# Kernel tuning notes

Measured on AMD Instinct MI355X. Metric: run time of the kernel, lower is better.

The kernel has to match this reference:

```python
import jax, jax.numpy as jnp
import numpy as np

N, E, HEADS = 50000, 800000, 4
IN_C, HID_C, OUT_C = 128, 64, 40
WIDTH = HEADS * HID_C  # 256
NEG_SLOPE = 0.2
BN_EPS = 1e-5


def setup_inputs() -> dict:
    key = jax.random.key(0)
    ks = jax.random.split(key, 16)
    s = 0.05
    inp = {
        "x": jax.random.normal(ks[0], (N, IN_C), jnp.float32),
        "edge_index": jax.random.randint(ks[1], (2, E), 0, N, jnp.int32),
        # layer 0: in -> (heads, hid), concat
        "W0": jax.random.normal(ks[2], (IN_C, WIDTH), jnp.float32) * s,
        "a_src0": jax.random.normal(ks[3], (HEADS, HID_C), jnp.float32) * s,
        "a_dst0": jax.random.normal(ks[4], (HEADS, HID_C), jnp.float32) * s,
        "b0": jnp.zeros((WIDTH,), jnp.float32),
        "g0": jnp.ones((WIDTH,), jnp.float32),
        "beta0": jnp.zeros((WIDTH,), jnp.float32),
        # layer 1: width -> (heads, hid), concat
        "W1": jax.random.normal(ks[5], (WIDTH, WIDTH), jnp.float32) * s,
        "a_src1": jax.random.normal(ks[6], (HEADS, HID_C), jnp.float32) * s,
        "a_dst1": jax.random.normal(ks[7], (HEADS, HID_C), jnp.float32) * s,
        "b1": jnp.zeros((WIDTH,), jnp.float32),
        "g1": jnp.ones((WIDTH,), jnp.float32),
        "beta1": jnp.zeros((WIDTH,), jnp.float32),
        # layer 2: width -> (heads, out), mean over heads (concat=False)
        "W2": jax.random.normal(ks[8], (WIDTH, HEADS * OUT_C), jnp.float32) * s,
        "a_src2": jax.random.normal(ks[9], (HEADS, OUT_C), jnp.float32) * s,
        "a_dst2": jax.random.normal(ks[10], (HEADS, OUT_C), jnp.float32) * s,
        "b2": jnp.zeros((OUT_C,), jnp.float32),
    }
    return inp


def _gat_layer(x, W, a_src, a_dst, b, src, dst, out_c, concat):
    # x: [N, F_in]; W: [F_in, HEADS*out_c]
    h = (x @ W).reshape(N, HEADS, out_c)              # [N, H, C]
    e_src = jnp.sum(h * a_src, axis=-1)               # [N, H]
    e_dst = jnp.sum(h * a_dst, axis=-1)               # [N, H]
    e = jax.nn.leaky_relu(e_src[src] + e_dst[dst], NEG_SLOPE)  # [E', H]
    # segment softmax over incoming edges of each destination node
    m = jax.ops.segment_max(e, dst, num_segments=N)
    e = jnp.exp(e - m[dst])
    z = jax.ops.segment_sum(e, dst, num_segments=N)
    alpha = e / (z[dst] + 1e-16)                      # [E', H]
    msg = h[src] * alpha[:, :, None]                  # [E', H, C]
    out = jax.ops.segment_sum(msg, dst, num_segments=N)  # [N, H, C]
    if concat:
        return out.reshape(N, HEADS * out_c) + b
    return out.mean(axis=1) + b


def _batchnorm(x, g, beta):
    mu = x.mean(axis=0)
    var = x.var(axis=0)
    return (x - mu) * jax.lax.rsqrt(var + BN_EPS) * g + beta


def reference(x, edge_index, W0, a_src0, a_dst0, b0, g0, beta0,
              W1, a_src1, a_dst1, b1, g1, beta1,
              W2, a_src2, a_dst2, b2):
    # add self-loops (PyG GATConv default)
    loops = jnp.arange(N, dtype=edge_index.dtype)
    src = jnp.concatenate([edge_index[0], loops])
    dst = jnp.concatenate([edge_index[1], loops])

    h = _gat_layer(x, W0, a_src0, a_dst0, b0, src, dst, HID_C, True)
    h = jax.nn.elu(_batchnorm(h, g0, beta0))
    h = _gat_layer(h, W1, a_src1, a_dst1, b1, src, dst, HID_C, True)
    h = jax.nn.elu(_batchnorm(h, g1, beta1))
    h = _gat_layer(h, W2, a_src2, a_dst2, b2, src, dst, OUT_C, False)
    return jax.nn.log_softmax(h, axis=-1)
```

## Files before the change

kernel.cpp:

```cpp
#include <hip/hip_runtime.h>

#define NN 50000
#define EE 800000
#define NEP (EE + NN)
#define NBS 512
#define SCB 49

typedef float f32x4 __attribute__((ext_vector_type(4)));
typedef float f32x2 __attribute__((ext_vector_type(2)));
typedef short bf16x8 __attribute__((ext_vector_type(8)));

__device__ inline float bf2f(unsigned short u) {
    union { unsigned int i; float f; } v; v.i = ((unsigned int)u) << 16; return v.f;
}
__device__ inline float lo2f(unsigned int u) {
    return __builtin_bit_cast(float, u << 16);
}
__device__ inline float hi2f(unsigned int u) {
    return __builtin_bit_cast(float, u & 0xFFFF0000u);
}
__device__ inline unsigned short f2bf(float f) {
    unsigned int x = __builtin_bit_cast(unsigned int, f);
    unsigned int r = x + 0x7FFFu + ((x >> 16) & 1u);
    return (unsigned short)(r >> 16);
}

#define XN4 1600000
#define GPREP 6826
#define GEDGE 3321
#define GWAVE 12500
#define GMAT  782

__global__ __launch_bounds__(256) void k_prep(const float* __restrict__ x, unsigned short* __restrict__ xb,
        const float* __restrict__ W0, unsigned short* __restrict__ Wt0,
        const float* __restrict__ W1, unsigned short* __restrict__ Wt1,
        const float* __restrict__ W2, unsigned short* __restrict__ Wt2,
        const float* __restrict__ vs0, const float* __restrict__ vd0,
        float4* __restrict__ es4, float4* __restrict__ ed4,
        const int* __restrict__ ei, int* __restrict__ counts, int* __restrict__ lps) {
    if (blockIdx.x >= GPREP) {
        int e = (blockIdx.x - GPREP) * 256 + threadIdx.x;
        if (e >= NEP) return;
        int dst = (e < EE) ? ei[EE + e] : (e - EE);
        lps[e] = atomicAdd(&counts[dst], 1);
        return;
    }
    int i = blockIdx.x * 256 + threadIdx.x;
    if (i < XN4) {
        float4 v = ((const float4*)x)[i];
        ushort4 o;
        o.x = f2bf(v.x); o.y = f2bf(v.y); o.z = f2bf(v.z); o.w = f2bf(v.w);
        ((ushort4*)xb)[i] = o;
        const int k0 = (i & 31) * 4;
        const float vv[4] = {v.x, v.y, v.z, v.w};
        float s[4] = {0.f, 0.f, 0.f, 0.f}, dd[4] = {0.f, 0.f, 0.f, 0.f};
        #pragma unroll
        for (int j = 0; j < 4; j++) {
            float f = vv[j];
            float4 a = *(const float4*)&vs0[(k0 + j) * 4];
            float4 b = *(const float4*)&vd0[(k0 + j) * 4];
            s[0] += f * a.x; s[1] += f * a.y; s[2] += f * a.z; s[3] += f * a.w;
            dd[0] += f * b.x; dd[1] += f * b.y; dd[2] += f * b.z; dd[3] += f * b.w;
        }
        #pragma unroll
        for (int d = 1; d < 32; d <<= 1) {
            #pragma unroll
            for (int j = 0; j < 4; j++) { s[j] += __shfl_xor(s[j], d); dd[j] += __shfl_xor(dd[j], d); }
        }
        if ((threadIdx.x & 31) == 0) {
            int row = i >> 5;
            es4[row] = make_float4(s[0], s[1], s[2], s[3]);
            ed4[row] = make_float4(dd[0], dd[1], dd[2], dd[3]);
        }
        return;
    }
    i -= XN4;
    if (i < 256 * 128) {
        int c = i >> 7, k = i & 127;
        Wt0[i] = f2bf(W0[(size_t)k * 256 + c]);
        return;
    }
    i -= 256 * 128;
    if (i < 256 * 256) {
        int c = i >> 8, k = i & 255;
        Wt1[i] = f2bf(W1[(size_t)k * 256 + c]);
        return;
    }
    i -= 256 * 256;
    if (i < 192 * 256) {
        int c = i >> 8, k = i & 255;
        Wt2[i] = f2bf((c < 160) ? W2[(size_t)k * 160 + c] : 0.f);
    }
}

__global__ __launch_bounds__(256) void k_scan1(const int* __restrict__ counts,
                                               int* __restrict__ indptr, int* __restrict__ bsum) {
    const int tid = threadIdx.x, lane = tid & 63, wid = tid >> 6;
    const int base = blockIdx.x * 1024 + tid * 4;
    int4 v = make_int4(0, 0, 0, 0);
    if (base + 3 < NN) v = *(const int4*)&counts[base];
    else {
        if (base + 0 < NN) v.x = counts[base + 0];
        if (base + 1 < NN) v.y = counts[base + 1];
        if (base + 2 < NN) v.z = counts[base + 2];
        if (base + 3 < NN) v.w = counts[base + 3];
    }
    int t = v.x + v.y + v.z + v.w;
    int s = t;
    #pragma unroll
    for (int d = 1; d < 64; d <<= 1) { int u = __shfl_up(s, d); if (lane >= d) s += u; }
    __shared__ int ws[4], wo[4];
    if (lane == 63) ws[wid] = s;
    __syncthreads();
    if (tid == 0) {
        int a = 0;
        #pragma unroll
        for (int j = 0; j < 4; j++) { wo[j] = a; a += ws[j]; }
        bsum[blockIdx.x] = a;
    }
    __syncthreads();
    int excl = wo[wid] + s - t;
    int p0 = excl, p1 = p0 + v.x, p2 = p1 + v.y, p3 = p2 + v.z;
    if (base + 3 < NN) *(int4*)&indptr[base] = make_int4(p0, p1, p2, p3);
    else {
        if (base + 0 < NN) indptr[base + 0] = p0;
        if (base + 1 < NN) indptr[base + 1] = p1;
        if (base + 2 < NN) indptr[base + 2] = p2;
        if (base + 3 < NN) indptr[base + 3] = p3;
    }
}

__global__ __launch_bounds__(64) void k_scan2(int* __restrict__ bsum, int* __restrict__ indptr) {
    const int lane = threadIdx.x;
    int v = (lane < SCB) ? bsum[lane] : 0;
    int s = v;
    #pragma unroll
    for (int d = 1; d < 64; d <<= 1) { int u = __shfl_up(s, d); if (lane >= d) s += u; }
    if (lane < SCB) bsum[lane] = s - v;
    if (lane == SCB - 1) indptr[NN] = s;
}

__global__ __launch_bounds__(256) void k_scan3(int* __restrict__ indptr, const int* __restrict__ bsum) {
    const int base = blockIdx.x * 1024 + threadIdx.x * 4;
    const int off = bsum[blockIdx.x];
    if (off == 0) return;
    if (base + 3 < NN) {
        int4 v = *(const int4*)&indptr[base];
        v.x += off; v.y += off; v.z += off; v.w += off;
        *(int4*)&indptr[base] = v;
    } else {
        #pragma unroll
        for (int j = 0; j < 4; j++)
            if (base + j < NN) indptr[base + j] += off;
    }
}

__global__ __launch_bounds__(256) void k_place(const int* __restrict__ ei,
                                               const int* __restrict__ indptr,
                                               const int* __restrict__ lps,
                                               int* __restrict__ srcs,
                                               int* __restrict__ dstc) {
    if (blockIdx.x < GEDGE) {
        int e = blockIdx.x * 256 + threadIdx.x;
        if (e >= NEP) return;
        int src, dst;
        if (e < EE) { src = ei[e]; dst = ei[EE + e]; }
        else        { src = e - EE; dst = src; }
        srcs[indptr[dst] + lps[e]] = src;
        return;
    }
    const int wid = threadIdx.x >> 6, lane = threadIdx.x & 63;
    const int n = (blockIdx.x - GEDGE) * 4 + wid;
    if (n >= NN) return;
    const int e0 = __builtin_amdgcn_readfirstlane(indptr[n]);
    const int e1 = __builtin_amdgcn_readfirstlane(indptr[n + 1]);
    for (int e = e0 + lane; e < e1; e += 64) dstc[e] = n;
}

__global__ __launch_bounds__(256) void k_wv(
        const float* __restrict__ W0, const float* __restrict__ as0, const float* __restrict__ ad0,
        const float* __restrict__ W1, const float* __restrict__ as1, const float* __restrict__ ad1,
        const float* __restrict__ W2, const float* __restrict__ as2, const float* __restrict__ ad2,
        float* __restrict__ vs0, float* __restrict__ vd0,
        float* __restrict__ vs1, float* __restrict__ vd1,
        float* __restrict__ vs2, float* __restrict__ vd2) {
    int b = blockIdx.x;
    const float *W, *as_, *ad_; float *vs, *vd; int k, C, NO;
    if (b < 128)      { W = W0; as_ = as0; ad_ = ad0; vs = vs0; vd = vd0; k = b;       C = 64; NO = 256; }
    else if (b < 384) { W = W1; as_ = as1; ad_ = ad1; vs = vs1; vd = vd1; k = b - 128; C = 64; NO = 256; }
    else              { W = W2; as_ = as2; ad_ = ad2; vs = vs2; vd = vd2; k = b - 384; C = 40; NO = 160; }
    int h = threadIdx.x >> 6, c = threadIdx.x & 63;
    float s1 = 0.f, s2 = 0.f;
    if (c < C) {
        float wv = W[(size_t)k * NO + h * C + c];
        s1 = wv * as_[h * C + c];
        s2 = wv * ad_[h * C + c];
    }
    #pragma unroll
    for (int d = 1; d < 64; d <<= 1) { s1 += __shfl_xor(s1, d); s2 += __shfl_xor(s2, d); }
    if (c == 0) { vs[k * 4 + h] = s1; vd[k * 4 + h] = s2; }
}

template<int K, int NOUTP, int NO>
__global__ __launch_bounds__(256) void k_gemm(const unsigned short* __restrict__ Xb,
                                              const unsigned short* __restrict__ Wt,
                                              unsigned char* __restrict__ Y,
                                              const float4* __restrict__ es4,
                                              const float4* __restrict__ ed4,
                                              const int* __restrict__ srcs,
                                              const int* __restrict__ dstc,
                                              uint2* __restrict__ wq) {
    if (blockIdx.x >= GMAT) {
        int p = (blockIdx.x - GMAT) * 256 + threadIdx.x;
        if (p >= NEP) return;
        float4 s = es4[srcs[p]];
        float4 d = ed4[dstc[p]];
        float e0 = s.x + d.x, e1 = s.y + d.y, e2 = s.z + d.z, e3 = s.w + d.w;
        e0 = (e0 > 0.f) ? e0 : 0.2f * e0;
        e1 = (e1 > 0.f) ? e1 : 0.2f * e1;
        e2 = (e2 > 0.f) ? e2 : 0.2f * e2;
        e3 = (e3 > 0.f) ? e3 : 0.2f * e3;
        uint2 o;
        o.x = (unsigned int)f2bf(__expf(e0)) | ((unsigned int)f2bf(__expf(e1)) << 16);
        o.y = (unsigned int)f2bf(__expf(e2)) | ((unsigned int)f2bf(__expf(e3)) << 16);
        wq[p] = o;
        return;
    }
    constexpr int G = K / 8;
    __shared__ __attribute__((aligned(16))) unsigned short As[64 * K];
    const int bm = blockIdx.x * 64;
    const int tid = threadIdx.x, lane = tid & 63, wid = tid >> 6;
    const int wm = wid >> 1, wn = wid & 1;
    const int l15 = lane & 15, l4 = lane >> 4;

    #pragma unroll
    for (int i = 0; i < (64 * G) / 256; i++) {
        int p = tid + 256 * i;
        int row = p / G, g = p % G;
        int grow = bm + row; if (grow >= NN) grow = 0;
        int gsrc = g ^ (row & 7);
        const unsigned short* gp = &Xb[(size_t)grow * K + gsrc * 8];
        __builtin_amdgcn_global_load_lds(
            (const __attribute__((address_space(1))) void*)gp,
            (__attribute__((address_space(3))) void*)&As[p * 8],
            16, 0, 0);
    }
    __syncthreads();

    #pragma unroll
    for (int bg = 0; bg < NOUTP / 64; bg++) {
        const int bn = bg * 64;
        bf16x8 bfr[2][K / 32];
        #pragma unroll
        for (int n = 0; n < 2; n++) {
            const int col = bn + wn * 32 + n * 16 + l15;
            #pragma unroll
            for (int ks = 0; ks < K / 32; ks++)
                bfr[n][ks] = *(const bf16x8*)&Wt[(size_t)col * K + ks * 32 + l4 * 8];
        }
        f32x4 acc[2][2];
        #pragma unroll
        for (int m = 0; m < 2; m++)
            #pragma unroll
            for (int n = 0; n < 2; n++) acc[m][n] = (f32x4)0.f;
        #pragma unroll
        for (int ks = 0; ks < K / 32; ks++) {
            #pragma unroll
            for (int m = 0; m < 2; m++) {
                const int r = wm * 32 + m * 16 + l15;
                const int pg = ((ks << 2) + l4) ^ (r & 7);
                bf16x8 af = *(const bf16x8*)&As[r * K + pg * 8];
                #pragma unroll
                for (int n = 0; n < 2; n++)
                    acc[m][n] = __builtin_amdgcn_mfma_f32_16x16x32_bf16(af, bfr[n][ks], acc[m][n], 0, 0, 0);
            }
        }
        #pragma unroll
        for (int m = 0; m < 2; m++) {
            const int row0 = bm + wm * 32 + m * 16 + l4 * 4;
            #pragma unroll
            for (int n = 0; n < 2; n++) {
                const int col = bn + wn * 32 + n * 16 + l15;
                if (col >= NO) continue;
                #pragma unroll
                for (int j = 0; j < 4; j++) {
                    int gr = row0 + j;
                    if (gr >= NN) continue;
                    int pk = __builtin_amdgcn_cvt_pk_fp8_f32(acc[m][n][j], acc[m][n][j], 0, false);
                    Y[(size_t)gr * NOUTP + col] = (unsigned char)pk;
                }
            }
        }
    }
}

__global__ __launch_bounds__(256) void k_agg(const unsigned char* __restrict__ H,
        const uint2* __restrict__ wq,
        const int* __restrict__ indptr, const int* __restrict__ srcs,
        unsigned short* __restrict__ outp) {
    const int wid = threadIdx.x >> 6, lane = threadIdx.x & 63;
    const int n = blockIdx.x * 4 + wid;
    if (n >= NN) return;
    const int head = lane >> 4;
    const int hw = head >> 1, hs = (head & 1) * 16;
    const int e0 = __builtin_amdgcn_readfirstlane(indptr[n]);
    const int e1 = __builtin_amdgcn_readfirstlane(indptr[n + 1]);
    float z = 0.f, a0 = 0.f, a1 = 0.f, a2 = 0.f, a3 = 0.f;
    const unsigned char* Hp = H + lane * 4;
    int e = e0;
    for (; e + 8 <= e1; e += 8) {
        int s[8]; float ww[8];
        #pragma unroll
        for (int q = 0; q < 8; q++) {
            s[q] = srcs[e + q];
            uint2 w2 = wq[e + q];
            unsigned int wsv = hw ? w2.y : w2.x;
            ww[q] = bf2f((unsigned short)(wsv >> hs));
        }
        #pragma unroll
        for (int q = 0; q < 8; q++) {
            unsigned int hv = *(const unsigned int*)(Hp + (size_t)s[q] * 256);
            z += ww[q];
            f32x2 lo = __builtin_amdgcn_cvt_pk_f32_fp8(hv, false);
            f32x2 hi = __builtin_amdgcn_cvt_pk_f32_fp8(hv, true);
            a0 += ww[q] * lo[0]; a1 += ww[q] * lo[1];
            a2 += ww[q] * hi[0]; a3 += ww[q] * hi[1];
        }
    }
    for (; e < e1; ++e) {
        int s0 = srcs[e];
        uint2 w2 = wq[e];
        unsigned int wsv = hw ? w2.y : w2.x;
        float w0 = bf2f((unsigned short)(wsv >> hs));
        unsigned int hv = *(const unsigned int*)(Hp + (size_t)s0 * 256);
        z += w0;
        f32x2 lo = __builtin_amdgcn_cvt_pk_f32_fp8(hv, false);
        f32x2 hi = __builtin_amdgcn_cvt_pk_f32_fp8(hv, true);
        a0 += w0 * lo[0]; a1 += w0 * lo[1];
        a2 += w0 * hi[0]; a3 += w0 * hi[1];
    }
    float inv = 1.f / (z + 1e-16f);
    ushort4 o;
    o.x = f2bf(a0 * inv); o.y = f2bf(a1 * inv); o.z = f2bf(a2 * inv); o.w = f2bf(a3 * inv);
    *(ushort4*)&outp[(size_t)n * 256 + lane * 4] = o;
}

__global__ __launch_bounds__(256) void k_agg2(const unsigned char* __restrict__ H2,
        const uint2* __restrict__ wq,
        const int* __restrict__ indptr, const int* __restrict__ srcs,
        const float* __restrict__ b2, float* __restrict__ outp) {
    const int wid = threadIdx.x >> 6, lane = threadIdx.x & 63;
    const int n = blockIdx.x * 4 + wid;
    if (n >= NN) return;
    const bool act = lane < 40;
    const int head = lane / 10;
    const int hw = head >> 1, hs = (head & 1) * 16;
    const int e0 = __builtin_amdgcn_readfirstlane(indptr[n]);
    const int e1 = __builtin_amdgcn_readfirstlane(indptr[n + 1]);
    float z = 0.f, acc[4] = {0.f, 0.f, 0.f, 0.f};
    const unsigned char* Hp = H2 + lane * 4;
    if (act) {
        int e = e0;
        for (; e + 8 <= e1; e += 8) {
            int s[8]; float ww[8];
            #pragma unroll
            for (int q = 0; q < 8; q++) {
                s[q] = srcs[e + q];
                uint2 w2 = wq[e + q];
                unsigned int wsv = hw ? w2.y : w2.x;
                ww[q] = bf2f((unsigned short)(wsv >> hs));
            }
            #pragma unroll
            for (int q = 0; q < 8; q++) {
                unsigned int hv = *(const unsigned int*)(Hp + (size_t)s[q] * 192);
                z += ww[q];
                f32x2 lo = __builtin_amdgcn_cvt_pk_f32_fp8(hv, false);
                f32x2 hi = __builtin_amdgcn_cvt_pk_f32_fp8(hv, true);
                acc[0] += ww[q] * lo[0]; acc[1] += ww[q] * lo[1];
                acc[2] += ww[q] * hi[0]; acc[3] += ww[q] * hi[1];
            }
        }
        for (; e < e1; ++e) {
            int s0 = srcs[e];
            uint2 w2 = wq[e];
            unsigned int wsv = hw ? w2.y : w2.x;
            float w0 = bf2f((unsigned short)(wsv >> hs));
            unsigned int hv = *(const unsigned int*)(Hp + (size_t)s0 * 192);
            z += w0;
            f32x2 lo = __builtin_amdgcn_cvt_pk_f32_fp8(hv, false);
            f32x2 hi = __builtin_amdgcn_cvt_pk_f32_fp8(hv, true);
            acc[0] += w0 * lo[0]; acc[1] += w0 * lo[1];
            acc[2] += w0 * hi[0]; acc[3] += w0 * hi[1];
        }
    }
    float inv = 1.f / (z + 1e-16f);
    float sv[4];
    #pragma unroll
    for (int j = 0; j < 4; j++) sv[j] = acc[j] * inv;
    #pragma unroll
    for (int j = 0; j < 4; j++) {
        float v = sv[j];
        v += __shfl(sv[j], lane + 10);
        v += __shfl(sv[j], lane + 20);
        v += __shfl(sv[j], lane + 30);
        sv[j] = v;
    }
    const bool ol = lane < 10;
    float m4 = -1e30f;
    #pragma unroll
    for (int j = 0; j < 4; j++) {
        sv[j] = ol ? (0.25f * sv[j] + b2[lane * 4 + j]) : -1e30f;
        m4 = fmaxf(m4, sv[j]);
    }
    #pragma unroll
    for (int d = 1; d < 16; d <<= 1) m4 = fmaxf(m4, __shfl_xor(m4, d));
    float s = 0.f;
    #pragma unroll
    for (int j = 0; j < 4; j++) s += ol ? __expf(sv[j] - m4) : 0.f;
    #pragma unroll
    for (int d = 1; d < 16; d <<= 1) s += __shfl_xor(s, d);
    float ls = logf(s);
    if (ol) {
        float4 o = make_float4(sv[0] - m4 - ls, sv[1] - m4 - ls, sv[2] - m4 - ls, sv[3] - m4 - ls);
        *(float4*)&outp[(size_t)n * 40 + lane * 4] = o;
    }
}

__global__ __launch_bounds__(256) void k_bnstats1(const unsigned short* __restrict__ X,
        float* __restrict__ ps, float* __restrict__ pq) {
    __shared__ float lds[4 * 256];
    const int tid = threadIdx.x;
    const int colg = (tid & 63) * 4;
    const int w = tid >> 6;
    float s[4] = {0.f, 0.f, 0.f, 0.f}, q[4] = {0.f, 0.f, 0.f, 0.f};
    for (int r = blockIdx.x * 4 + w; r < NN; r += NBS * 4) {
        ushort4 hv = *(const ushort4*)&X[(size_t)r * 256 + colg];
        const unsigned short hh[4] = {hv.x, hv.y, hv.z, hv.w};
        #pragma unroll
        for (int j = 0; j < 4; j++) { float v = bf2f(hh[j]); s[j] += v; q[j] += v * v; }
    }
    #pragma unroll
    for (int j = 0; j < 4; j++) lds[w * 256 + colg + j] = s[j];
    __syncthreads();
    float ts = lds[tid] + lds[256 + tid] + lds[512 + tid] + lds[768 + tid];
    __syncthreads();
    #pragma unroll
    for (int j = 0; j < 4; j++) lds[w * 256 + colg + j] = q[j];
    __syncthreads();
    float tq = lds[tid] + lds[256 + tid] + lds[512 + tid] + lds[768 + tid];
    ps[(size_t)blockIdx.x * 256 + tid] = ts;
    pq[(size_t)blockIdx.x * 256 + tid] = tq;
}

__global__ __launch_bounds__(256) void k_bnred(const float* __restrict__ ps,
        const float* __restrict__ pq, const float* __restrict__ g,
        const float* __restrict__ beta, float* __restrict__ sc_o, float* __restrict__ sh_o) {
    const int col = blockIdx.x, tid = threadIdx.x;
    float s = ps[(size_t)tid * 256 + col] + ps[(size_t)(tid + 256) * 256 + col];
    float q = pq[(size_t)tid * 256 + col] + pq[(size_t)(tid + 256) * 256 + col];
    #pragma unroll
    for (int d = 1; d < 64; d <<= 1) { s += __shfl_xor(s, d); q += __shfl_xor(q, d); }
    __shared__ float ls[4], lq[4];
    if ((tid & 63) == 0) { ls[tid >> 6] = s; lq[tid >> 6] = q; }
    __syncthreads();
    if (tid == 0) {
        float S = ls[0] + ls[1] + ls[2] + ls[3];
        float Q = lq[0] + lq[1] + lq[2] + lq[3];
        const float inv = 1.f / (float)NN;
        float mu = S * inv;
        float var = Q * inv - mu * mu;
        float sc = rsqrtf(var + 1e-5f) * g[col];
        sc_o[col] = sc;
        sh_o[col] = beta[col] - mu * sc;
    }
}

__global__ __launch_bounds__(256) void k_bnapply(unsigned short* __restrict__ X,
        const float* __restrict__ sc_i, const float* __restrict__ sh_i,
        const float* __restrict__ vs, const float* __restrict__ vd,
        float4* __restrict__ es4, float4* __restrict__ ed4) {
    const int hl = threadIdx.x & 31;
    const int colg = hl * 8;
    const int rowo = threadIdx.x >> 5;
    float sc[8], sh[8];
    #pragma unroll
    for (int j = 0; j < 8; j++) { sc[j] = sc_i[colg + j]; sh[j] = sh_i[colg + j]; }
    for (int r = blockIdx.x * 8 + rowo; r < NN; r += gridDim.x * 8) {
        uint4 u = *(uint4*)&X[(size_t)r * 256 + colg];
        unsigned int uu[4] = {u.x, u.y, u.z, u.w};
        unsigned int oo[4];
        float s[4] = {0.f, 0.f, 0.f, 0.f}, dd[4] = {0.f, 0.f, 0.f, 0.f};
        #pragma unroll
        for (int p = 0; p < 4; p++) {
            float lo = lo2f(uu[p]);
            float hi = hi2f(uu[p]);
            float vlo = lo * sc[p * 2] + sh[p * 2];
            float vhi = hi * sc[p * 2 + 1] + sh[p * 2 + 1];
            vlo = (vlo > 0.f) ? vlo : expm1f(vlo);
            vhi = (vhi > 0.f) ? vhi : expm1f(vhi);
            oo[p] = (unsigned int)f2bf(vlo) | ((unsigned int)f2bf(vhi) << 16);
            float4 a0 = *(const float4*)&vs[(colg + 2 * p) * 4];
            float4 b0 = *(const float4*)&vd[(colg + 2 * p) * 4];
            float4 a1 = *(const float4*)&vs[(colg + 2 * p + 1) * 4];
            float4 b1 = *(const float4*)&vd[(colg + 2 * p + 1) * 4];
            s[0] += vlo * a0.x + vhi * a1.x; s[1] += vlo * a0.y + vhi * a1.y;
            s[2] += vlo * a0.z + vhi * a1.z; s[3] += vlo * a0.w + vhi * a1.w;
            dd[0] += vlo * b0.x + vhi * b1.x; dd[1] += vlo * b0.y + vhi * b1.y;
            dd[2] += vlo * b0.z + vhi * b1.z; dd[3] += vlo * b0.w + vhi * b1.w;
        }
        *(uint4*)&X[(size_t)r * 256 + colg] = make_uint4(oo[0], oo[1], oo[2], oo[3]);
        #pragma unroll
        for (int d = 1; d < 32; d <<= 1) {
            #pragma unroll
            for (int j = 0; j < 4; j++) { s[j] += __shfl_xor(s[j], d); dd[j] += __shfl_xor(dd[j], d); }
        }
        if (hl == 0) {
            es4[r] = make_float4(s[0], s[1], s[2], s[3]);
            ed4[r] = make_float4(dd[0], dd[1], dd[2], dd[3]);
        }
    }
}

extern "C" void kernel_launch(void* const* d_in, const int* in_sizes, int n_in,
                              void* d_out, int out_size, void* d_ws, size_t ws_size,
                              hipStream_t stream) {
    const float* x   = (const float*)d_in[0];
    const int*   ei  = (const int*)d_in[1];
    const float* W0  = (const float*)d_in[2];
    const float* as0 = (const float*)d_in[3];
    const float* ad0 = (const float*)d_in[4];
    const float* g0  = (const float*)d_in[6];
    const float* be0 = (const float*)d_in[7];
    const float* W1  = (const float*)d_in[8];
    const float* as1 = (const float*)d_in[9];
    const float* ad1 = (const float*)d_in[10];
    const float* g1  = (const float*)d_in[12];
    const float* be1 = (const float*)d_in[13];
    const float* W2  = (const float*)d_in[14];
    const float* as2 = (const float*)d_in[15];
    const float* ad2 = (const float*)d_in[16];
    const float* b2  = (const float*)d_in[17];
    float* out = (float*)d_out;

    char* w = (char*)d_ws;
    size_t off = 0;
    auto take = [&](size_t bytes) -> void* {
        off = (off + 255) & ~(size_t)255;
        void* p = w + off; off += bytes; return p;
    };
    unsigned short* Agg16 = (unsigned short*)take((size_t)NN * 256 * 2);
    unsigned short* xb    = (unsigned short*)take((size_t)NN * 128 * 2);
    unsigned char*  H8    = (unsigned char*)take((size_t)NN * 256);
    float* es     = (float*)take((size_t)NN * 4 * 4);
    float* ed     = (float*)take((size_t)NN * 4 * 4);
    int*   counts = (int*)take((size_t)NN * 4);
    int*   indptr = (int*)take((size_t)(NN + 1) * 4);
    int*   lps    = (int*)take((size_t)NEP * 4);
    int*   srcs   = (int*)take((size_t)NEP * 4);
    int*   dstc   = (int*)take((size_t)NEP * 4);
    uint2* wq     = (uint2*)take((size_t)NEP * 8);
    int*   bsum   = (int*)take(64 * 4);
    unsigned short* Wt0 = (unsigned short*)take((size_t)256 * 128 * 2);
    unsigned short* Wt1 = (unsigned short*)take((size_t)256 * 256 * 2);
    unsigned short* Wt2 = (unsigned short*)take((size_t)192 * 256 * 2);
    float* vs0 = (float*)take(128 * 4 * 4);
    float* vd0 = (float*)take(128 * 4 * 4);
    float* vs1 = (float*)take(256 * 4 * 4);
    float* vd1 = (float*)take(256 * 4 * 4);
    float* vs2 = (float*)take(256 * 4 * 4);
    float* vd2 = (float*)take(256 * 4 * 4);
    float* ps  = (float*)take((size_t)NBS * 256 * 4);
    float* pq  = (float*)take((size_t)NBS * 256 * 4);
    float* bns = (float*)take(512 * 4);

    k_wv<<<640, 256, 0, stream>>>(W0, as0, ad0, W1, as1, ad1, W2, as2, ad2,
                                  vs0, vd0, vs1, vd1, vs2, vd2);
    hipMemsetAsync(counts, 0, (size_t)NN * 4, stream);
    k_prep<<<GPREP + GEDGE, 256, 0, stream>>>(x, xb, W0, Wt0, W1, Wt1, W2, Wt2,
                                              vs0, vd0, (float4*)es, (float4*)ed,
                                              ei, counts, lps);
    k_scan1<<<SCB, 256, 0, stream>>>(counts, indptr, bsum);
    k_scan2<<<1, 64, 0, stream>>>(bsum, indptr);
    k_scan3<<<SCB, 256, 0, stream>>>(indptr, bsum);
    k_place<<<GEDGE + GWAVE, 256, 0, stream>>>(ei, indptr, lps, srcs, dstc);

    k_gemm<128, 256, 256><<<GMAT + GEDGE, 256, 0, stream>>>(xb, Wt0, H8,
            (const float4*)es, (const float4*)ed, srcs, dstc, wq);
    k_agg<<<GWAVE, 256, 0, stream>>>(H8, wq, indptr, srcs, Agg16);
    k_bnstats1<<<NBS, 256, 0, stream>>>(Agg16, ps, pq);
    k_bnred<<<256, 256, 0, stream>>>(ps, pq, g0, be0, bns, bns + 256);
    k_bnapply<<<1024, 256, 0, stream>>>(Agg16, bns, bns + 256, vs1, vd1,
                                        (float4*)es, (float4*)ed);

    k_gemm<256, 256, 256><<<GMAT + GEDGE, 256, 0, stream>>>(Agg16, Wt1, H8,
            (const float4*)es, (const float4*)ed, srcs, dstc, wq);
    k_agg<<<GWAVE, 256, 0, stream>>>(H8, wq, indptr, srcs, Agg16);
    k_bnstats1<<<NBS, 256, 0, stream>>>(Agg16, ps, pq);
    k_bnred<<<256, 256, 0, stream>>>(ps, pq, g1, be1, bns, bns + 256);
    k_bnapply<<<1024, 256, 0, stream>>>(Agg16, bns, bns + 256, vs2, vd2,
                                        (float4*)es, (float4*)ed);

    k_gemm<256, 192, 160><<<GMAT + GEDGE, 256, 0, stream>>>(Agg16, Wt2, H8,
            (const float4*)es, (const float4*)ed, srcs, dstc, wq);
    k_agg2<<<GWAVE, 256, 0, stream>>>(H8, wq, indptr, srcs, b2, out);
}
```

Measured before the change: 352.2 us.

## Move edge counting into layer-0 GEMM and split out edge weight kernel

The atomic in-degree counting pass moves from the prep kernel into the layer-0 GEMM launch, which now runs before the CSR scan and placement. This lets the dense GEMM overlap the atomic counting work instead of the conversion prep. Layer-0 edge attention weights, which need the CSR arrays, are now computed in a new standalone kernel after placement. The change adds one kernel launch and may shift load balance between the GEMM blocks and the atomic blocks.

```diff
diff --git a/kernel.cpp b/kernel.cpp
--- a/kernel.cpp
+++ b/kernel.cpp
@@ -36,15 +36,7 @@
         const float* __restrict__ W1, unsigned short* __restrict__ Wt1,
         const float* __restrict__ W2, unsigned short* __restrict__ Wt2,
         const float* __restrict__ vs0, const float* __restrict__ vd0,
-        float4* __restrict__ es4, float4* __restrict__ ed4,
-        const int* __restrict__ ei, int* __restrict__ counts, int* __restrict__ lps) {
-    if (blockIdx.x >= GPREP) {
-        int e = (blockIdx.x - GPREP) * 256 + threadIdx.x;
-        if (e >= NEP) return;
-        int dst = (e < EE) ? ei[EE + e] : (e - EE);
-        lps[e] = atomicAdd(&counts[dst], 1);
-        return;
-    }
+        float4* __restrict__ es4, float4* __restrict__ ed4) {
     int i = blockIdx.x * 256 + threadIdx.x;
     if (i < XN4) {
         float4 v = ((const float4*)x)[i];
@@ -175,6 +167,24 @@
     const int e0 = __builtin_amdgcn_readfirstlane(indptr[n]);
     const int e1 = __builtin_amdgcn_readfirstlane(indptr[n + 1]);
     for (int e = e0 + lane; e < e1; e += 64) dstc[e] = n;
+}
+
+__global__ __launch_bounds__(256) void k_wgt(const float4* __restrict__ es4,
+        const float4* __restrict__ ed4, const int* __restrict__ srcs,
+        const int* __restrict__ dstc, uint2* __restrict__ wq) {
+    int p = blockIdx.x * 256 + threadIdx.x;
+    if (p >= NEP) return;
+    float4 s = es4[srcs[p]];
+    float4 d = ed4[dstc[p]];
+    float e0 = s.x + d.x, e1 = s.y + d.y, e2 = s.z + d.z, e3 = s.w + d.w;
+    e0 = (e0 > 0.f) ? e0 : 0.2f * e0;
+    e1 = (e1 > 0.f) ? e1 : 0.2f * e1;
+    e2 = (e2 > 0.f) ? e2 : 0.2f * e2;
+    e3 = (e3 > 0.f) ? e3 : 0.2f * e3;
+    uint2 o;
+    o.x = (unsigned int)f2bf(__expf(e0)) | ((unsigned int)f2bf(__expf(e1)) << 16);
+    o.y = (unsigned int)f2bf(__expf(e2)) | ((unsigned int)f2bf(__expf(e3)) << 16);
+    wq[p] = o;
 }
 
 __global__ __launch_bounds__(256) void k_wv(
@@ -201,7 +211,7 @@
     if (c == 0) { vs[k * 4 + h] = s1; vd[k * 4 + h] = s2; }
 }
 
-template<int K, int NOUTP, int NO>
+template<int K, int NOUTP, int NO, bool CSPASS>
 __global__ __launch_bounds__(256) void k_gemm(const unsigned short* __restrict__ Xb,
                                               const unsigned short* __restrict__ Wt,
                                               unsigned char* __restrict__ Y,
@@ -209,21 +219,29 @@
                                               const float4* __restrict__ ed4,
                                               const int* __restrict__ srcs,
                                               const int* __restrict__ dstc,
-                                              uint2* __restrict__ wq) {
+                                              uint2* __restrict__ wq,
+                                              const int* __restrict__ ei,
+                                              int* __restrict__ counts,
+                                              int* __restrict__ lps) {
     if (blockIdx.x >= GMAT) {
         int p = (blockIdx.x - GMAT) * 256 + threadIdx.x;
         if (p >= NEP) return;
-        float4 s = es4[srcs[p]];
-        float4 d = ed4[dstc[p]];
-        float e0 = s.x + d.x, e1 = s.y + d.y, e2 = s.z + d.z, e3 = s.w + d.w;
-        e0 = (e0 > 0.f) ? e0 : 0.2f * e0;
-        e1 = (e1 > 0.f) ? e1 : 0.2f * e1;
-        e2 = (e2 > 0.f) ? e2 : 0.2f * e2;
-        e3 = (e3 > 0.f) ? e3 : 0.2f * e3;
-        uint2 o;
-        o.x = (unsigned int)f2bf(__expf(e0)) | ((unsigned int)f2bf(__expf(e1)) << 16);
-        o.y = (unsigned int)f2bf(__expf(e2)) | ((unsigned int)f2bf(__expf(e3)) << 16);
-        wq[p] = o;
+        if constexpr (CSPASS) {
+            int dst = (p < EE) ? ei[EE + p] : (p - EE);
+            lps[p] = atomicAdd(&counts[dst], 1);
+        } else {
+            float4 s = es4[srcs[p]];
+            float4 d = ed4[dstc[p]];
+            float e0 = s.x + d.x, e1 = s.y + d.y, e2 = s.z + d.z, e3 = s.w + d.w;
+            e0 = (e0 > 0.f) ? e0 : 0.2f * e0;
+            e1 = (e1 > 0.f) ? e1 : 0.2f * e1;
+            e2 = (e2 > 0.f) ? e2 : 0.2f * e2;
+            e3 = (e3 > 0.f) ? e3 : 0.2f * e3;
+            uint2 o;
+            o.x = (unsigned int)f2bf(__expf(e0)) | ((unsigned int)f2bf(__expf(e1)) << 16);
+            o.y = (unsigned int)f2bf(__expf(e2)) | ((unsigned int)f2bf(__expf(e3)) << 16);
+            wq[p] = o;
+        }
         return;
     }
     constexpr int G = K / 8;
@@ -576,31 +594,33 @@
     k_wv<<<640, 256, 0, stream>>>(W0, as0, ad0, W1, as1, ad1, W2, as2, ad2,
                                   vs0, vd0, vs1, vd1, vs2, vd2);
     hipMemsetAsync(counts, 0, (size_t)NN * 4, stream);
-    k_prep<<<GPREP + GEDGE, 256, 0, stream>>>(x, xb, W0, Wt0, W1, Wt1, W2, Wt2,
-                                              vs0, vd0, (float4*)es, (float4*)ed,
-                                              ei, counts, lps);
+    k_prep<<<GPREP, 256, 0, stream>>>(x, xb, W0, Wt0, W1, Wt1, W2, Wt2,
+                                      vs0, vd0, (float4*)es, (float4*)ed);
+
+    k_gemm<128, 256, 256, true><<<GMAT + GEDGE, 256, 0, stream>>>(xb, Wt0, H8,
+            nullptr, nullptr, nullptr, nullptr, nullptr, ei, counts, lps);
+
     k_scan1<<<SCB, 256, 0, stream>>>(counts, indptr, bsum);
     k_scan2<<<1, 64, 0, stream>>>(bsum, indptr);
     k_scan3<<<SCB, 256, 0, stream>>>(indptr, bsum);
     k_place<<<GEDGE + GWAVE, 256, 0, stream>>>(ei, indptr, lps, srcs, dstc);
-
-    k_gemm<128, 256, 256><<<GMAT + GEDGE, 256, 0, stream>>>(xb, Wt0, H8,
-            (const float4*)es, (const float4*)ed, srcs, dstc, wq);
+    k_wgt<<<GEDGE, 256, 0, stream>>>((const float4*)es, (const float4*)ed, srcs, dstc, wq);
+
     k_agg<<<GWAVE, 256, 0, stream>>>(H8, wq, indptr, srcs, Agg16);
     k_bnstats1<<<NBS, 256, 0, stream>>>(Agg16, ps, pq);
     k_bnred<<<256, 256, 0, stream>>>(ps, pq, g0, be0, bns, bns + 256);
     k_bnapply<<<1024, 256, 0, stream>>>(Agg16, bns, bns + 256, vs1, vd1,
                                         (float4*)es, (float4*)ed);
 
-    k_gemm<256, 256, 256><<<GMAT + GEDGE, 256, 0, stream>>>(Agg16, Wt1, H8,
-            (const float4*)es, (const float4*)ed, srcs, dstc, wq);
+    k_gemm<256, 256, 256, false><<<GMAT + GEDGE, 256, 0, stream>>>(Agg16, Wt1, H8,
+            (const float4*)es, (const float4*)ed, srcs, dstc, wq, nullptr, nullptr, nullptr);
     k_agg<<<GWAVE, 256, 0, stream>>>(H8, wq, indptr, srcs, Agg16);
     k_bnstats1<<<NBS, 256, 0, stream>>>(Agg16, ps, pq);
     k_bnred<<<256, 256, 0, stream>>>(ps, pq, g1, be1, bns, bns + 256);
     k_bnapply<<<1024, 256, 0, stream>>>(Agg16, bns, bns + 256, vs2, vd2,
                                         (float4*)es, (float4*)ed);
 
-    k_gemm<256, 192, 160><<<GMAT + GEDGE, 256, 0, stream>>>(Agg16, Wt2, H8,
-            (const float4*)es, (const float4*)ed, srcs, dstc, wq);
+    k_gemm<256, 192, 160, false><<<GMAT + GEDGE, 256, 0, stream>>>(Agg16, Wt2, H8,
+            (const float4*)es, (const float4*)ed, srcs, dstc, wq, nullptr, nullptr, nullptr);
     k_agg2<<<GWAVE, 256, 0, stream>>>(H8, wq, indptr, srcs, b2, out);
 }
```

Result: faster. 343.8 us (-2.4%).
